# Performance work log

Hardware: AMD Instinct MI355X
Metric: run time of the kernel (lower is better)

## Reference

```python
import jax, jax.numpy as jnp
import numpy as np

B, L, D = 2, 2048, 512
H, HD = 8, 64          # num_heads, head_dim (hidden_dim = 512)
WINDOW = 256
SCALE = float(np.sqrt(HD))
LN_EPS = 1e-5


def setup_inputs() -> dict:
    key = jax.random.key(0)
    ks = jax.random.split(key, 10)
    sequence = jax.random.normal(ks[0], (B, L, D), dtype=jnp.float32)
    # lengths in [L - WINDOW//2, L] so no query row is fully masked (avoids NaN, matches original's valid regime)
    sequence_lengths = jax.random.randint(ks[1], (B,), L - WINDOW // 2, L + 1, dtype=jnp.int32)
    timestamps = jnp.sort(jax.random.uniform(ks[2], (B, L), dtype=jnp.float32) * float(L), axis=-1)
    w_std = 0.02
    Wq = jax.random.normal(ks[3], (H * HD, D), dtype=jnp.float32) * w_std
    Wk = jax.random.normal(ks[4], (H * HD, D), dtype=jnp.float32) * w_std
    Wv = jax.random.normal(ks[5], (H * HD, D), dtype=jnp.float32) * w_std
    Wo = jax.random.normal(ks[6], (D, H * HD), dtype=jnp.float32) * w_std
    bo = jnp.zeros((D,), dtype=jnp.float32)
    ln_gamma = jnp.ones((D,), dtype=jnp.float32)
    ln_beta = jnp.zeros((D,), dtype=jnp.float32)
    temporal_weight = jnp.array([0.1], dtype=jnp.float32)
    return {
        "sequence": sequence, "sequence_lengths": sequence_lengths, "timestamps": timestamps,
        "ln_gamma": ln_gamma, "ln_beta": ln_beta,
        "Wq": Wq, "Wk": Wk, "Wv": Wv, "Wo": Wo, "bo": bo,
        "temporal_weight": temporal_weight,
    }


def reference(sequence, sequence_lengths, timestamps, ln_gamma, ln_beta,
              Wq, Wk, Wv, Wo, bo, temporal_weight):
    residual = sequence
    # LayerNorm over input_dim
    mu = jnp.mean(sequence, axis=-1, keepdims=True)
    var = jnp.mean(jnp.square(sequence - mu), axis=-1, keepdims=True)
    x = (sequence - mu) * jax.lax.rsqrt(var + LN_EPS) * ln_gamma + ln_beta

    # QKV projections (spectral-normalized Linear, no bias) -> [B, L, H, HD]
    Q = (x @ Wq.T).reshape(B, L, H, HD)
    K = (x @ Wk.T).reshape(B, L, H, HD)
    V = (x @ Wv.T).reshape(B, L, H, HD)

    scores = jnp.einsum("bqhd,bkhd->bhqk", Q, K) / SCALE  # [B, H, L, L]

    # temporal decay bias
    ts_diff = jnp.abs(timestamps[:, :, None] - timestamps[:, None, :])  # [B, L, L]
    temporal_weights = jnp.exp(-jnp.abs(temporal_weight[0]) * ts_diff)
    scores = scores + jnp.log(temporal_weights + 1e-8)[:, None, :, :]

    neg_inf = jnp.float32(-jnp.inf)
    # sliding window mask (L > window_size): |i - j| <= window_size // 2
    idx = jnp.arange(L)
    wmask = jnp.abs(idx[None, :] - idx[:, None]) <= WINDOW // 2  # [L, L]
    scores = jnp.where(wmask[None, None, :, :], scores, neg_inf)

    # padding mask on key positions
    pmask = idx[None, :] < sequence_lengths[:, None]  # [B, L]
    scores = jnp.where(pmask[:, None, None, :], scores, neg_inf)

    attn = jax.nn.softmax(scores, axis=-1)  # [B, H, L, L]
    attended = jnp.einsum("bhqk,bkhd->bqhd", attn, V).reshape(B, L, H * HD)

    output = attended @ Wo.T + bo + residual  # [B, L, D]

    # exponential position-weighted aggregation over valid positions
    pos = idx.astype(jnp.float32)
    pw = jnp.exp(-0.1 * (L - 1 - pos))[None, :] * pmask.astype(jnp.float32)  # [B, L]
    pw = pw / (jnp.sum(pw, axis=1, keepdims=True) + 1e-8)
    aggregated = jnp.sum(output * pw[:, :, None], axis=1)  # [B, D]
    return aggregated
```

## Files before the change

### kernel.cpp

```cpp
#include <hip/hip_runtime.h>
#include <math.h>

#define B 2
#define L 2048
#define D 512
#define H 8
#define HD 64
#define W2 128
#define NOUT (3*D)

#define QS 1792
#define NQ (L - QS)
#define ROWS0 (QS - W2)
#define NROWS (L - ROWS0)
#define MROWS (B * NROWS)

#define TQ 4
#define NQT (NQ / TQ)

typedef __bf16 bf16_t;
typedef __attribute__((ext_vector_type(4))) __bf16 bf16x4;
typedef __attribute__((ext_vector_type(8))) __bf16 bf16x8;
typedef __attribute__((ext_vector_type(4))) float f32x4;

#define PREP_LN_BLOCKS (MROWS / 4)
#define PREP_CVT_BLOCKS 768
#define PREP_AGGS_BLOCKS 64
#define PREP_GRID (PREP_LN_BLOCKS + PREP_CVT_BLOCKS + PREP_AGGS_BLOCKS)

__global__ __launch_bounds__(256) void prep_kernel(const float* __restrict__ seq,
                                                   const float* __restrict__ gamma,
                                                   const float* __restrict__ beta,
                                                   const float* __restrict__ Wq,
                                                   const float* __restrict__ Wk,
                                                   const float* __restrict__ Wv,
                                                   const int* __restrict__ slen,
                                                   bf16_t* __restrict__ xb,
                                                   bf16_t* __restrict__ wb,
                                                   float* __restrict__ aggS) {
    int blk = blockIdx.x;
    int tid = threadIdx.x;
    int wid = tid >> 6, lane = tid & 63;

    if (blk < PREP_LN_BLOCKS) {
        int row = blk * 4 + wid;
        int b = row / NROWS;
        int l = ROWS0 + (row - b * NROWS);
        const float* src = seq + ((size_t)b * L + l) * D;
        float4 v0 = ((const float4*)src)[lane];
        float4 v1 = ((const float4*)src)[lane + 64];
        float s  = v0.x + v0.y + v0.z + v0.w + v1.x + v1.y + v1.z + v1.w;
        float sq = v0.x*v0.x + v0.y*v0.y + v0.z*v0.z + v0.w*v0.w
                 + v1.x*v1.x + v1.y*v1.y + v1.z*v1.z + v1.w*v1.w;
        for (int o = 32; o; o >>= 1) { s += __shfl_xor(s, o); sq += __shfl_xor(sq, o); }
        float mu = s * (1.0f / D);
        float var = sq * (1.0f / D) - mu * mu;
        float rstd = rsqrtf(var + 1e-5f);
        float4 g0 = ((const float4*)gamma)[lane];
        float4 g1 = ((const float4*)gamma)[lane + 64];
        float4 b0 = ((const float4*)beta)[lane];
        float4 b1 = ((const float4*)beta)[lane + 64];
        bf16x4 c0, c1;
        c0[0] = (bf16_t)((v0.x - mu) * rstd * g0.x + b0.x);
        c0[1] = (bf16_t)((v0.y - mu) * rstd * g0.y + b0.y);
        c0[2] = (bf16_t)((v0.z - mu) * rstd * g0.z + b0.z);
        c0[3] = (bf16_t)((v0.w - mu) * rstd * g0.w + b0.w);
        c1[0] = (bf16_t)((v1.x - mu) * rstd * g1.x + b1.x);
        c1[1] = (bf16_t)((v1.y - mu) * rstd * g1.y + b1.y);
        c1[2] = (bf16_t)((v1.z - mu) * rstd * g1.z + b1.z);
        c1[3] = (bf16_t)((v1.w - mu) * rstd * g1.w + b1.w);
        bf16x4* dst = (bf16x4*)(xb + (size_t)row * D);
        dst[lane] = c0;
        dst[lane + 64] = c1;
    } else if (blk < PREP_LN_BLOCKS + PREP_CVT_BLOCKS) {
        int idx = (blk - PREP_LN_BLOCKS) * 256 + tid;
        const float* src = (idx < 65536) ? Wq : (idx < 131072 ? Wk : Wv);
        int off = idx & 65535;
        float4 v = ((const float4*)src)[off];
        bf16x4 o;
        o[0] = (bf16_t)v.x; o[1] = (bf16_t)v.y; o[2] = (bf16_t)v.z; o[3] = (bf16_t)v.w;
        ((bf16x4*)wb)[idx] = o;
    } else {
        int idx = blk - (PREP_LN_BLOCKS + PREP_CVT_BLOCKS);
        int b = idx >> 5;
        int rc = (idx >> 3) & 3;
        int ct = idx & 7;
        int col = ct * 64 + lane;
        int nv = slen[b] - QS;
        int i0 = rc * 64 + wid * 16;
        int i1 = min(i0 + 16, nv);
        float s2 = 0.f;
#pragma unroll 4
        for (int i = i0; i < i1; ++i) {
            s2 += __expf(-0.1f * (float)(NQ - 1 - i)) * seq[((size_t)(b * L + QS + i)) * D + col];
        }
        if (i1 > i0) atomicAdd(&aggS[b * D + col], s2);
    }
}

__global__ __launch_bounds__(256) void qkv_gemm(const bf16_t* __restrict__ xb,
                                                const bf16_t* __restrict__ wb,
                                                bf16_t* __restrict__ Qb,
                                                bf16_t* __restrict__ Kb,
                                                bf16_t* __restrict__ Vb) {
    int m0 = blockIdx.x * 32, n0 = blockIdx.y * 64;
    int wid = threadIdx.x >> 6, lane = threadIdx.x & 63;
    int mw = m0 + (wid >> 1) * 16;
    int nw = n0 + (wid & 1) * 32;
    int mr = lane & 15, quad = lane >> 4;
    f32x4 acc0 = {}, acc1 = {};
    const bf16_t* aptr = xb + (size_t)(mw + mr) * D + quad * 8;
    const bf16_t* bptr = wb + (size_t)(nw + mr) * D + quad * 8;
#pragma unroll 8
    for (int k = 0; k < D; k += 32) {
        bf16x8 a  = *(const bf16x8*)(aptr + k);
        bf16x8 b0 = *(const bf16x8*)(bptr + k);
        bf16x8 b1 = *(const bf16x8*)(bptr + 16 * D + k);
        acc0 = __builtin_amdgcn_mfma_f32_16x16x32_bf16(a, b0, acc0, 0, 0, 0);
        acc1 = __builtin_amdgcn_mfma_f32_16x16x32_bf16(a, b1, acc1, 0, 0, 0);
    }
    int sec = n0 >> 9;
    int h = (n0 >> 6) & 7;
    int d0 = nw & 63;
    bf16_t* dstbase = (sec == 0) ? Qb : (sec == 1 ? Kb : Vb);
    int m = mw + quad * 4;
    int b = m / NROWS;
    int r = m - b * NROWS;
    bf16_t* dst = dstbase + ((size_t)(b * H + h) * NROWS + r) * HD + d0 + mr;
#pragma unroll
    for (int rr = 0; rr < 4; ++rr) {
        dst[(size_t)rr * HD]      = (bf16_t)acc0[rr];
        dst[(size_t)rr * HD + 16] = (bf16_t)acc1[rr];
    }
}

__global__ __launch_bounds__(256) void attn_kernel(const bf16_t* __restrict__ Qb,
                                                   const bf16_t* __restrict__ Kb,
                                                   const bf16_t* __restrict__ Vb,
                                                   const float* __restrict__ ts,
                                                   const int* __restrict__ slen,
                                                   const float* __restrict__ tw,
                                                   float* __restrict__ aggA) {
    int bid = blockIdx.x;
    int b = bid / (NQT * H);
    int rem = bid - b * (NQT * H);
    int qt = rem / H;
    int h = rem - qt * H;
    int wid = threadIdx.x >> 6;
    int lane = threadIdx.x & 63;
    int q0 = QS + qt * TQ;
    int sl = slen[b];
    if (q0 >= sl) return;
    int kmin = q0 - W2;
    int kmax = min(q0 + TQ - 1 + W2, sl - 1);
    int nk = kmax - kmin + 1;
    int chunk = (nk + 3) >> 2;
    int start = wid * chunk;
    int end = min(start + chunk, nk);
    int cnt = max(end - start, 0);

    __shared__ __attribute__((aligned(16))) float qv[TQ][HD];
    __shared__ __attribute__((aligned(16))) float p[4][66][TQ];
    __shared__ __attribute__((aligned(16))) float pacc[4][TQ][HD];
    __shared__ float mlm[4][TQ];
    __shared__ float mll[4][TQ];
    __shared__ float tqs[TQ];

    const size_t headbase = (size_t)(b * H + h) * NROWS;

    {
        int qr = q0 + wid - ROWS0;
        qv[wid][lane] = (float)Qb[(headbase + qr) * HD + lane];
        if (lane == 0) tqs[wid] = ts[b * L + q0 + wid];
    }
    __syncthreads();

    float atw = fabsf(tw[0]);

    float m[TQ] = {-INFINITY, -INFINITY, -INFINITY, -INFINITY};
    float sreg[2][TQ];
#pragma unroll
    for (int it = 0; it < 2; ++it) {
        int kk = start + it * 64 + lane;
        bool act = (kk < end);
        float s[TQ] = {0.f, 0.f, 0.f, 0.f};
        if (act) {
            int k = kmin + kk;
            const bf16_t* Krow = Kb + (headbase + (k - ROWS0)) * HD;
#pragma unroll
            for (int d8 = 0; d8 < 8; ++d8) {
                bf16x8 kv = *(const bf16x8*)(Krow + d8 * 8);
                float kf0 = (float)kv[0], kf1 = (float)kv[1], kf2 = (float)kv[2], kf3 = (float)kv[3];
                float kf4 = (float)kv[4], kf5 = (float)kv[5], kf6 = (float)kv[6], kf7 = (float)kv[7];
#pragma unroll
                for (int t = 0; t < TQ; ++t) {
                    const float* qq = &qv[t][d8 * 8];
                    s[t] += qq[0]*kf0 + qq[1]*kf1 + qq[2]*kf2 + qq[3]*kf3
                          + qq[4]*kf4 + qq[5]*kf5 + qq[6]*kf6 + qq[7]*kf7;
                }
            }
            float tk = ts[b * L + k];
#pragma unroll
            for (int t = 0; t < TQ; ++t) {
                float dt = fabsf(tqs[t] - tk);
                float bias = logf(expf(-atw * dt) + 1e-8f);
                int qa = q0 + t;
                bool valid = (k >= qa - W2) && (k <= qa + W2);
                s[t] = valid ? (s[t] * 0.125f + bias) : -INFINITY;
            }
        } else {
#pragma unroll
            for (int t = 0; t < TQ; ++t) s[t] = -INFINITY;
        }
#pragma unroll
        for (int t = 0; t < TQ; ++t) { sreg[it][t] = s[t]; m[t] = fmaxf(m[t], s[t]); }
    }
#pragma unroll
    for (int t = 0; t < TQ; ++t)
        for (int o = 32; o; o >>= 1) m[t] = fmaxf(m[t], __shfl_xor(m[t], o));

    float l[TQ] = {0.f, 0.f, 0.f, 0.f};
#pragma unroll
    for (int it = 0; it < 2; ++it) {
        int kk = start + it * 64 + lane;
        bool act = (kk < end);
        float pv[TQ];
#pragma unroll
        for (int t = 0; t < TQ; ++t) {
            float pp = (m[t] > -INFINITY) ? expf(sreg[it][t] - m[t]) : 0.0f;
            pv[t] = pp;
            l[t] += act ? pp : 0.0f;
        }
        if (act) {
            *(float4*)&p[wid][kk - start][0] = make_float4(pv[0], pv[1], pv[2], pv[3]);
        }
    }
#pragma unroll
    for (int t = 0; t < TQ; ++t)
        for (int o = 32; o; o >>= 1) l[t] += __shfl_xor(l[t], o);
    if (lane == 0) {
#pragma unroll
        for (int t = 0; t < TQ; ++t) { mlm[wid][t] = m[t]; mll[wid][t] = l[t]; }
    }

    float acc[TQ] = {0.f, 0.f, 0.f, 0.f};
    const bf16_t* Vbase = Vb + (headbase + (kmin + start - ROWS0)) * HD + lane;
#pragma unroll 4
    for (int kl = 0; kl < cnt; ++kl) {
        float v = (float)Vbase[(size_t)kl * HD];
        float4 pp = *(const float4*)&p[wid][kl][0];
        acc[0] += pp.x * v; acc[1] += pp.y * v; acc[2] += pp.z * v; acc[3] += pp.w * v;
    }
#pragma unroll
    for (int t = 0; t < TQ; ++t) pacc[wid][t][lane] = acc[t];
    __syncthreads();

    {
        int t = wid;
        int q = q0 + t;
        if (q < sl) {
            float m0 = mlm[0][t], m1 = mlm[1][t], m2 = mlm[2][t], m3 = mlm[3][t];
            float M = fmaxf(fmaxf(m0, m1), fmaxf(m2, m3));
            float e0 = expf(m0 - M), e1 = expf(m1 - M), e2 = expf(m2 - M), e3 = expf(m3 - M);
            float Lsum = e0 * mll[0][t] + e1 * mll[1][t] + e2 * mll[2][t] + e3 * mll[3][t];
            float o = e0 * pacc[0][t][lane] + e1 * pacc[1][t][lane]
                    + e2 * pacc[2][t][lane] + e3 * pacc[3][t][lane];
            float wq = __expf(-0.1f * (float)(L - 1 - q));
            atomicAdd(&aggA[b * D + h * HD + lane], (o / Lsum) * wq);
        }
    }
}

__global__ __launch_bounds__(64) void out_kernel(const float* __restrict__ aggA,
                                                 const float* __restrict__ aggS,
                                                 const float* __restrict__ Wo,
                                                 const float* __restrict__ bo,
                                                 const int* __restrict__ slen,
                                                 float* __restrict__ out) {
    int bid = blockIdx.x;
    int b = bid >> 9;
    int d = bid & 511;
    int lane = threadIdx.x;
    int nv = slen[b] - QS;
    float den = 0.f;
#pragma unroll
    for (int j = 0; j < 4; ++j) {
        int i = lane * 4 + j;
        den += (i < nv) ? __expf(-0.1f * (float)(NQ - 1 - i)) : 0.0f;
    }
    for (int o = 32; o; o >>= 1) den += __shfl_xor(den, o);

    const float* wrow = Wo + (size_t)d * D;
    const float* arow = aggA + b * D;
    float acc = 0.0f;
#pragma unroll
    for (int i = 0; i < 8; ++i) {
        int j = lane + 64 * i;
        acc += arow[j] * wrow[j];
    }
    for (int o = 32; o; o >>= 1) acc += __shfl_xor(acc, o);
    if (lane == 0) {
        float inv = 1.0f / (den + 1e-8f);
        out[b * D + d] = (acc + aggS[b * D + d] + bo[d] * den) * inv;
    }
}

extern "C" void kernel_launch(void* const* d_in, const int* in_sizes, int n_in,
                              void* d_out, int out_size, void* d_ws, size_t ws_size,
                              hipStream_t stream) {
    const float* seq   = (const float*)d_in[0];
    const int*   slen  = (const int*)d_in[1];
    const float* ts    = (const float*)d_in[2];
    const float* gamma = (const float*)d_in[3];
    const float* beta  = (const float*)d_in[4];
    const float* Wq    = (const float*)d_in[5];
    const float* Wk    = (const float*)d_in[6];
    const float* Wv    = (const float*)d_in[7];
    const float* Wo    = (const float*)d_in[8];
    const float* bo    = (const float*)d_in[9];
    const float* tw    = (const float*)d_in[10];
    float* out = (float*)d_out;

    float* ws    = (float*)d_ws;
    float* aggA  = ws;
    float* aggS  = aggA + B * D;
    bf16_t* xb   = (bf16_t*)(aggS + B * D);
    bf16_t* wb   = xb + (size_t)MROWS * D;
    bf16_t* Qb   = wb + (size_t)NOUT * D;
    bf16_t* Kb   = Qb + (size_t)B * H * NROWS * HD;
    bf16_t* Vb   = Kb + (size_t)B * H * NROWS * HD;

    hipMemsetAsync(aggA, 0, 2 * B * D * sizeof(float), stream);
    prep_kernel<<<PREP_GRID, 256, 0, stream>>>(seq, gamma, beta, Wq, Wk, Wv, slen,
                                               xb, wb, aggS);
    dim3 ggrid(MROWS / 32, NOUT / 64);
    qkv_gemm<<<ggrid, 256, 0, stream>>>(xb, wb, Qb, Kb, Vb);
    attn_kernel<<<B * NQT * H, 256, 0, stream>>>(Qb, Kb, Vb, ts, slen, tw, aggA);
    out_kernel<<<B * D, 64, 0, stream>>>(aggA, aggS, Wo, bo, slen, out);
}
```

Measured before the change: 119.9 us.

## Drop memset, double attention query tile, use fast math, merge batch outputs

Removes the hipMemsetAsync by zeroing the attention accumulator in an extra prep block. The aggS atomics become per-chunk partial sums reduced in the output kernel, which now handles both batches per block. The attention query tile grows from 4 to 8 rows, halving the block count and reusing each K/V load across more queries. Precise exp/log calls become fast intrinsics. In exchange the larger tile raises register pressure, and the intrinsics slightly change numerics.

After: 122.6 us. 2.3% more time.

```diff
diff --git a/kernel.cpp b/kernel.cpp
--- a/kernel.cpp
+++ b/kernel.cpp
@@ -15,7 +15,7 @@
 #define NROWS (L - ROWS0)
 #define MROWS (B * NROWS)
 
-#define TQ 4
+#define TQ 8
 #define NQT (NQ / TQ)
 
 typedef __bf16 bf16_t;
@@ -26,7 +26,7 @@
 #define PREP_LN_BLOCKS (MROWS / 4)
 #define PREP_CVT_BLOCKS 768
 #define PREP_AGGS_BLOCKS 64
-#define PREP_GRID (PREP_LN_BLOCKS + PREP_CVT_BLOCKS + PREP_AGGS_BLOCKS)
+#define PREP_GRID (PREP_LN_BLOCKS + PREP_CVT_BLOCKS + PREP_AGGS_BLOCKS + 1)
 
 __global__ __launch_bounds__(256) void prep_kernel(const float* __restrict__ seq,
                                                    const float* __restrict__ gamma,
@@ -37,7 +37,8 @@
                                                    const int* __restrict__ slen,
                                                    bf16_t* __restrict__ xb,
                                                    bf16_t* __restrict__ wb,
-                                                   float* __restrict__ aggS) {
+                                                   float* __restrict__ aggA,
+                                                   float* __restrict__ aggSp) {
     int blk = blockIdx.x;
     int tid = threadIdx.x;
     int wid = tid >> 6, lane = tid & 63;
@@ -80,7 +81,8 @@
         bf16x4 o;
         o[0] = (bf16_t)v.x; o[1] = (bf16_t)v.y; o[2] = (bf16_t)v.z; o[3] = (bf16_t)v.w;
         ((bf16x4*)wb)[idx] = o;
-    } else {
+    } else if (blk < PREP_LN_BLOCKS + PREP_CVT_BLOCKS + PREP_AGGS_BLOCKS) {
+        __shared__ float red[4][64];
         int idx = blk - (PREP_LN_BLOCKS + PREP_CVT_BLOCKS);
         int b = idx >> 5;
         int rc = (idx >> 3) & 3;
@@ -94,7 +96,14 @@
         for (int i = i0; i < i1; ++i) {
             s2 += __expf(-0.1f * (float)(NQ - 1 - i)) * seq[((size_t)(b * L + QS + i)) * D + col];
         }
-        if (i1 > i0) atomicAdd(&aggS[b * D + col], s2);
+        red[wid][lane] = s2;
+        __syncthreads();
+        if (wid == 0) {
+            aggSp[(size_t)rc * (B * D) + b * D + col] =
+                red[0][lane] + red[1][lane] + red[2][lane] + red[3][lane];
+        }
+    } else {
+        ((float4*)aggA)[tid] = make_float4(0.f, 0.f, 0.f, 0.f);
     }
 }
 
@@ -170,20 +179,24 @@
 
     {
         int qr = q0 + wid - ROWS0;
-        qv[wid][lane] = (float)Qb[(headbase + qr) * HD + lane];
-        if (lane == 0) tqs[wid] = ts[b * L + q0 + wid];
+        qv[wid][lane]     = (float)Qb[(headbase + qr) * HD + lane];
+        qv[wid + 4][lane] = (float)Qb[(headbase + qr + 4) * HD + lane];
+        if (threadIdx.x < TQ) tqs[threadIdx.x] = ts[b * L + q0 + threadIdx.x];
     }
     __syncthreads();
 
     float atw = fabsf(tw[0]);
 
-    float m[TQ] = {-INFINITY, -INFINITY, -INFINITY, -INFINITY};
-    float sreg[2][TQ];
+    float m[TQ], sreg[2][TQ];
+#pragma unroll
+    for (int t = 0; t < TQ; ++t) m[t] = -INFINITY;
 #pragma unroll
     for (int it = 0; it < 2; ++it) {
         int kk = start + it * 64 + lane;
         bool act = (kk < end);
-        float s[TQ] = {0.f, 0.f, 0.f, 0.f};
+        float s[TQ];
+#pragma unroll
+        for (int t = 0; t < TQ; ++t) s[t] = 0.f;
         if (act) {
             int k = kmin + kk;
             const bf16_t* Krow = Kb + (headbase + (k - ROWS0)) * HD;
@@ -203,7 +216,7 @@
 #pragma unroll
             for (int t = 0; t < TQ; ++t) {
                 float dt = fabsf(tqs[t] - tk);
-                float bias = logf(expf(-atw * dt) + 1e-8f);
+                float bias = __logf(__expf(-atw * dt) + 1e-8f);
                 int qa = q0 + t;
                 bool valid = (k >= qa - W2) && (k <= qa + W2);
                 s[t] = valid ? (s[t] * 0.125f + bias) : -INFINITY;
@@ -219,7 +232,9 @@
     for (int t = 0; t < TQ; ++t)
         for (int o = 32; o; o >>= 1) m[t] = fmaxf(m[t], __shfl_xor(m[t], o));
 
-    float l[TQ] = {0.f, 0.f, 0.f, 0.f};
+    float l[TQ];
+#pragma unroll
+    for (int t = 0; t < TQ; ++t) l[t] = 0.f;
 #pragma unroll
     for (int it = 0; it < 2; ++it) {
         int kk = start + it * 64 + lane;
@@ -227,12 +242,13 @@
         float pv[TQ];
 #pragma unroll
         for (int t = 0; t < TQ; ++t) {
-            float pp = (m[t] > -INFINITY) ? expf(sreg[it][t] - m[t]) : 0.0f;
+            float pp = (m[t] > -INFINITY) ? __expf(sreg[it][t] - m[t]) : 0.0f;
             pv[t] = pp;
             l[t] += act ? pp : 0.0f;
         }
         if (act) {
             *(float4*)&p[wid][kk - start][0] = make_float4(pv[0], pv[1], pv[2], pv[3]);
+            *(float4*)&p[wid][kk - start][4] = make_float4(pv[4], pv[5], pv[6], pv[7]);
         }
     }
 #pragma unroll
@@ -243,25 +259,30 @@
         for (int t = 0; t < TQ; ++t) { mlm[wid][t] = m[t]; mll[wid][t] = l[t]; }
     }
 
-    float acc[TQ] = {0.f, 0.f, 0.f, 0.f};
+    float acc[TQ];
+#pragma unroll
+    for (int t = 0; t < TQ; ++t) acc[t] = 0.f;
     const bf16_t* Vbase = Vb + (headbase + (kmin + start - ROWS0)) * HD + lane;
 #pragma unroll 4
     for (int kl = 0; kl < cnt; ++kl) {
         float v = (float)Vbase[(size_t)kl * HD];
-        float4 pp = *(const float4*)&p[wid][kl][0];
-        acc[0] += pp.x * v; acc[1] += pp.y * v; acc[2] += pp.z * v; acc[3] += pp.w * v;
+        float4 p0 = *(const float4*)&p[wid][kl][0];
+        float4 p1 = *(const float4*)&p[wid][kl][4];
+        acc[0] += p0.x * v; acc[1] += p0.y * v; acc[2] += p0.z * v; acc[3] += p0.w * v;
+        acc[4] += p1.x * v; acc[5] += p1.y * v; acc[6] += p1.z * v; acc[7] += p1.w * v;
     }
 #pragma unroll
     for (int t = 0; t < TQ; ++t) pacc[wid][t][lane] = acc[t];
     __syncthreads();
 
-    {
-        int t = wid;
+#pragma unroll
+    for (int half = 0; half < 2; ++half) {
+        int t = wid + half * 4;
         int q = q0 + t;
         if (q < sl) {
             float m0 = mlm[0][t], m1 = mlm[1][t], m2 = mlm[2][t], m3 = mlm[3][t];
             float M = fmaxf(fmaxf(m0, m1), fmaxf(m2, m3));
-            float e0 = expf(m0 - M), e1 = expf(m1 - M), e2 = expf(m2 - M), e3 = expf(m3 - M);
+            float e0 = __expf(m0 - M), e1 = __expf(m1 - M), e2 = __expf(m2 - M), e3 = __expf(m3 - M);
             float Lsum = e0 * mll[0][t] + e1 * mll[1][t] + e2 * mll[2][t] + e3 * mll[3][t];
             float o = e0 * pacc[0][t][lane] + e1 * pacc[1][t][lane]
                     + e2 * pacc[2][t][lane] + e3 * pacc[3][t][lane];
@@ -272,36 +293,39 @@
 }
 
 __global__ __launch_bounds__(64) void out_kernel(const float* __restrict__ aggA,
-                                                 const float* __restrict__ aggS,
+                                                 const float* __restrict__ aggSp,
                                                  const float* __restrict__ Wo,
                                                  const float* __restrict__ bo,
                                                  const int* __restrict__ slen,
                                                  float* __restrict__ out) {
-    int bid = blockIdx.x;
-    int b = bid >> 9;
-    int d = bid & 511;
+    int d = blockIdx.x;
     int lane = threadIdx.x;
-    int nv = slen[b] - QS;
-    float den = 0.f;
+    int nv0 = slen[0] - QS, nv1 = slen[1] - QS;
+    float den0 = 0.f, den1 = 0.f;
 #pragma unroll
     for (int j = 0; j < 4; ++j) {
         int i = lane * 4 + j;
-        den += (i < nv) ? __expf(-0.1f * (float)(NQ - 1 - i)) : 0.0f;
-    }
-    for (int o = 32; o; o >>= 1) den += __shfl_xor(den, o);
+        float w = __expf(-0.1f * (float)(NQ - 1 - i));
+        den0 += (i < nv0) ? w : 0.0f;
+        den1 += (i < nv1) ? w : 0.0f;
+    }
+    for (int o = 32; o; o >>= 1) { den0 += __shfl_xor(den0, o); den1 += __shfl_xor(den1, o); }
 
     const float* wrow = Wo + (size_t)d * D;
-    const float* arow = aggA + b * D;
-    float acc = 0.0f;
+    float acc0 = 0.0f, acc1 = 0.0f;
 #pragma unroll
     for (int i = 0; i < 8; ++i) {
         int j = lane + 64 * i;
-        acc += arow[j] * wrow[j];
-    }
-    for (int o = 32; o; o >>= 1) acc += __shfl_xor(acc, o);
+        float w = wrow[j];
+        acc0 += aggA[j] * w;
+        acc1 += aggA[D + j] * w;
+    }
+    for (int o = 32; o; o >>= 1) { acc0 += __shfl_xor(acc0, o); acc1 += __shfl_xor(acc1, o); }
     if (lane == 0) {
-        float inv = 1.0f / (den + 1e-8f);
-        out[b * D + d] = (acc + aggS[b * D + d] + bo[d] * den) * inv;
+        float s0 = aggSp[d]         + aggSp[B*D + d]         + aggSp[2*B*D + d]         + aggSp[3*B*D + d];
+        float s1 = aggSp[D + d]     + aggSp[B*D + D + d]     + aggSp[2*B*D + D + d]     + aggSp[3*B*D + D + d];
+        out[d]     = (acc0 + s0 + bo[d] * den0) / (den0 + 1e-8f);
+        out[D + d] = (acc1 + s1 + bo[d] * den1) / (den1 + 1e-8f);
     }
 }
 
@@ -323,18 +347,17 @@
 
     float* ws    = (float*)d_ws;
     float* aggA  = ws;
-    float* aggS  = aggA + B * D;
-    bf16_t* xb   = (bf16_t*)(aggS + B * D);
+    float* aggSp = aggA + B * D;
+    bf16_t* xb   = (bf16_t*)(aggSp + 4 * B * D);
     bf16_t* wb   = xb + (size_t)MROWS * D;
     bf16_t* Qb   = wb + (size_t)NOUT * D;
     bf16_t* Kb   = Qb + (size_t)B * H * NROWS * HD;
     bf16_t* Vb   = Kb + (size_t)B * H * NROWS * HD;
 
-    hipMemsetAsync(aggA, 0, 2 * B * D * sizeof(float), stream);
     prep_kernel<<<PREP_GRID, 256, 0, stream>>>(seq, gamma, beta, Wq, Wk, Wv, slen,
-                                               xb, wb, aggS);
+                                               xb, wb, aggA, aggSp);
     dim3 ggrid(MROWS / 32, NOUT / 64);
     qkv_gemm<<<ggrid, 256, 0, stream>>>(xb, wb, Qb, Kb, Vb);
     attn_kernel<<<B * NQT * H, 256, 0, stream>>>(Qb, Kb, Vb, ts, slen, tw, aggA);
-    out_kernel<<<B * D, 64, 0, stream>>>(aggA, aggS, Wo, bo, slen, out);
-}
+    out_kernel<<<D, 64, 0, stream>>>(aggA, aggSp, Wo, bo, slen, out);
+}
```
